# Performance work log

Hardware: AMD Instinct MI355X
Metric: run time of the kernel (lower is better)

## Reference

```python
import jax, jax.numpy as jnp
import numpy as np

B, N, R = 16, 512, 10
DE, DR, DOUT = 256, 64, 256

def setup_inputs() -> dict:
    key = jax.random.key(0)
    k1, k2, k3, k4 = jax.random.split(key, 4)
    node_features = jax.random.normal(k1, (B, N, DE), dtype=jnp.float32)
    relation_features = jax.random.normal(k2, (B, R, DR), dtype=jnp.float32)
    adj = jax.random.uniform(k3, (B, R, N, N), dtype=jnp.float32)
    in_dim = (DE + DR) * R
    bound = float(np.sqrt(6.0 / (in_dim + DOUT)))  # xavier_uniform
    W = jax.random.uniform(k4, (DOUT, in_dim), dtype=jnp.float32, minval=-bound, maxval=bound)
    bias = jnp.zeros((DOUT,), dtype=jnp.float32)
    return {"node_features": node_features, "relation_features": relation_features,
            "adj": adj, "W": W, "bias": bias}

def reference(node_features, relation_features, adj, W, bias):
    # adj: [B,R,N,N]; node_features: [B,N,De]; relation_features: [B,R,Dr]
    # Per relation r: bmm(adj[:,r], cat([node, rel_r broadcast], -1))
    # Node part: adj @ node_features for every relation at once.
    node_part = jnp.einsum('brnm,bmd->brnd', adj, node_features)      # [B,R,N,De]
    # Relation part: adj @ (rel_r repeated over rows) == rowsum(adj) * rel_r
    rel_part = adj.sum(axis=-1)[..., None] * relation_features[:, :, None, :]  # [B,R,N,Dr]
    supports = jnp.concatenate([node_part, rel_part], axis=-1)        # [B,R,N,De+Dr]
    supports = supports.transpose(0, 2, 1, 3).reshape(node_features.shape[0],
                                                      node_features.shape[1], -1)  # [B,N,R*(De+Dr)]
    return supports @ W.T + bias
```

## Files before the change

### kernel.cpp

```cpp
#include <hip/hip_runtime.h>
#include <stdint.h>

#define B_     16
#define N_     512
#define R_     10
#define DE_    256
#define DR_    64
#define DOUT_  256
#define INDIM_ 3200
#define BLK_   320
#define RN_    5120
#define SPLITS_ 4
#define CPS_    20

typedef __bf16          v8bf  __attribute__((ext_vector_type(8)));
typedef unsigned short  v8us  __attribute__((ext_vector_type(8)));
typedef unsigned short  v4us  __attribute__((ext_vector_type(4)));
typedef float           f32x4 __attribute__((ext_vector_type(4)));

static __device__ __forceinline__ unsigned short f2b(float f) {
  union { float f; unsigned u; } c; c.f = f;
  unsigned r = c.u + 0x7FFFu + ((c.u >> 16) & 1u);
  return (unsigned short)(r >> 16);
}

static __device__ __forceinline__ v8bf us2bf(v8us u) {
  union { v8us u; v8bf b; } c; c.u = u; return c.b;
}

static __device__ __forceinline__ void gl_lds16(const void* g, void* l) {
  __builtin_amdgcn_global_load_lds(
      (const __attribute__((address_space(1))) void*)g,
      (__attribute__((address_space(3))) void*)l, 16, 0, 0);
}

static __device__ __forceinline__ void waitv4() { asm volatile("s_waitcnt vmcnt(4)" ::: "memory"); }
static __device__ __forceinline__ void waitv0() { asm volatile("s_waitcnt vmcnt(0)" ::: "memory"); }
static __device__ __forceinline__ void waitl0() { asm volatile("s_waitcnt lgkmcnt(0)" ::: "memory"); }
#define SCHED0() __builtin_amdgcn_sched_barrier(0)

__global__ void prep_all(const float* __restrict__ nf, const float* __restrict__ W,
                         const float* __restrict__ rel,
                         unsigned short* __restrict__ nodeB,
                         unsigned short* __restrict__ WnB,
                         float* __restrict__ Uf) {
  const int bb = blockIdx.x;
  const int tid = threadIdx.x;
  if (bb < 256) {
    const size_t base = (size_t)bb * 8192;
#pragma unroll
    for (int p = 0; p < 4; ++p) {
      size_t off = base + (size_t)p * 2048 + (size_t)tid * 8;
      float4 x = *(const float4*)(nf + off);
      float4 y = *(const float4*)(nf + off + 4);
      v8us u;
      u[0] = f2b(x.x); u[1] = f2b(x.y); u[2] = f2b(x.z); u[3] = f2b(x.w);
      u[4] = f2b(y.x); u[5] = f2b(y.y); u[6] = f2b(y.z); u[7] = f2b(y.w);
      *(v8us*)(nodeB + off) = u;
    }
  } else if (bb < 896) {
    int idx = (bb - 256) * 1024 + tid * 4;
    int r = idx >> 16;
    int o = (idx >> 8) & 255;
    int d = idx & 255;
    float4 x = *(const float4*)(W + (size_t)o * INDIM_ + r * BLK_ + d);
    v4us u;
    u[0] = f2b(x.x); u[1] = f2b(x.y); u[2] = f2b(x.z); u[3] = f2b(x.w);
    *(v4us*)(WnB + idx) = u;
  } else {
    int idx = (bb - 896) * 256 + tid;
    int o  = idx & 255;
    int br = idx >> 8;
    int r  = br % R_;
    const float* rp = rel + (size_t)br * DR_;
    const float* wp = W + (size_t)o * INDIM_ + r * BLK_ + DE_;
    float v = 0.f;
#pragma unroll 8
    for (int d = 0; d < DR_; ++d) v += rp[d] * wp[d];
    Uf[idx] = v;
  }
}

__global__ void stageA_gemm(const unsigned short* __restrict__ nodeB,
                            const unsigned short* __restrict__ WnB,
                            const float* __restrict__ Uf,
                            unsigned short* __restrict__ Gp) {
  __shared__ unsigned short S[40960];
  unsigned short* NodeP = S;
  unsigned short* Wbuf  = S + 16384;
  unsigned short* Cb    = S + 32768;
  const int b  = blockIdx.x;
  const int o0 = blockIdx.y * 128;
  const int m0 = (blockIdx.z & 7) * 64;
  const int r0 = (blockIdx.z >> 3) * 5;
  const int tid  = threadIdx.x;
  const int lane = tid & 63;
  const int wave = tid >> 6;
  const int wm = wave >> 1, wn = wave & 1;
  const int quad = lane >> 4, l16 = lane & 15;
  const int srl = lane >> 3;
  const int skc = lane & 7;

  const unsigned short* Nb = nodeB + (size_t)b * (N_ * DE_);

#pragma unroll
  for (int p = 0; p < 4; ++p)
#pragma unroll
    for (int it = 0; it < 2; ++it) {
      int rowblk = it * 32 + wave * 8;
      int rl = rowblk + srl;
      int kc = skc ^ (rl & 7);
      gl_lds16(Nb + (size_t)(m0 + rl) * DE_ + p * 64 + kc * 8,
               NodeP + p * 4096 + rowblk * 64);
    }
  {
    const unsigned short* Wb = WnB + (size_t)r0 * (DOUT_ * DE_);
#pragma unroll
    for (int it = 0; it < 4; ++it) {
      int rowblk = it * 32 + wave * 8;
      int rl = rowblk + srl;
      int kc = skc ^ (rl & 7);
      gl_lds16(Wb + (size_t)(o0 + rl) * DE_ + kc * 8, Wbuf + rowblk * 64);
    }
  }
  __syncthreads();

  for (int rr = 0; rr < 5; ++rr) {
    const int r = r0 + rr;
    f32x4 acc[4][2];
#pragma unroll
    for (int i = 0; i < 4; ++i)
#pragma unroll
      for (int j = 0; j < 2; ++j) acc[i][j] = f32x4{0.f, 0.f, 0.f, 0.f};

#pragma unroll
    for (int t = 0; t < 4; ++t) {
      if (rr < 4 || t < 3) {
        const int nr = (t < 3) ? r : (r + 1);
        const int nt = (t < 3) ? (t + 1) : 0;
        const unsigned short* Wb = WnB + (size_t)nr * (DOUT_ * DE_);
        unsigned short* Wd = Wbuf + ((t + 1) & 1) * 8192;
#pragma unroll
        for (int it = 0; it < 4; ++it) {
          int rowblk = it * 32 + wave * 8;
          int rl = rowblk + srl;
          int kc = skc ^ (rl & 7);
          gl_lds16(Wb + (size_t)(o0 + rl) * DE_ + nt * 64 + kc * 8, Wd + rowblk * 64);
        }
      }
      const unsigned short* Wc = Wbuf + (t & 1) * 8192;
      const unsigned short* Np = NodeP + t * 4096;
#pragma unroll
      for (int ks = 0; ks < 2; ++ks) {
        const int kb = ks * 4;
        v8bf av[4], bv[2];
#pragma unroll
        for (int mi = 0; mi < 4; ++mi) {
          int m = wm * 64 + mi * 16 + l16;
          av[mi] = us2bf(*(const v8us*)(Wc + m * 64 + (((kb + quad) ^ (m & 7)) * 8)));
        }
#pragma unroll
        for (int ni = 0; ni < 2; ++ni) {
          int c = wn * 32 + ni * 16 + l16;
          bv[ni] = us2bf(*(const v8us*)(Np + c * 64 + (((kb + quad) ^ (c & 7)) * 8)));
        }
#pragma unroll
        for (int mi = 0; mi < 4; ++mi)
#pragma unroll
          for (int ni = 0; ni < 2; ++ni)
            acc[mi][ni] = __builtin_amdgcn_mfma_f32_16x16x32_bf16(av[mi], bv[ni], acc[mi][ni], 0, 0, 0);
      }
      __syncthreads();
    }

#pragma unroll
    for (int mi = 0; mi < 4; ++mi)
#pragma unroll
      for (int tt = 0; tt < 4; ++tt) {
        int o_loc = wm * 64 + mi * 16 + quad * 4 + tt;
        float u = Uf[((size_t)b * R_ + r) * DOUT_ + o0 + o_loc];
#pragma unroll
        for (int ni = 0; ni < 2; ++ni) {
          int m_loc = wn * 32 + ni * 16 + l16;
          Cb[o_loc * 64 + m_loc] = f2b(acc[mi][ni][tt] + u);
        }
      }
    __syncthreads();
#pragma unroll
    for (int p = 0; p < 4; ++p) {
      int idx16 = p * 2048 + tid * 8;
      int orow = idx16 >> 6;
      int moff = idx16 & 63;
      unsigned short* dst = Gp + ((size_t)(b * DOUT_ + o0 + orow)) * RN_ + r * N_ + m0 + moff;
      *(v8us*)dst = *(const v8us*)(Cb + idx16);
    }
    __syncthreads();
  }
}

__global__ __launch_bounds__(512, 1)
void stageB_gemm(const float* __restrict__ adj,
                 const unsigned short* __restrict__ Gp,
                 float* __restrict__ part) {
  __shared__ unsigned short SB[2 * 24576];
  const int b  = blockIdx.x;
  const int n0 = blockIdx.y * 128;
  const int sp = blockIdx.z;
  const int tid  = threadIdx.x;
  const int lane = tid & 63;
  const int wave = tid >> 6;
  const int wm = wave >> 2;
  const int wn = wave & 3;
  const int quad = lane >> 4, l16 = lane & 15;

  const float* Ab = adj + (size_t)b * (R_ * N_ * N_);
  const unsigned short* Gb = Gp + (size_t)b * (DOUT_ * RN_);

  f32x4 acc[4][4];
#pragma unroll
  for (int i = 0; i < 4; ++i)
#pragma unroll
    for (int j = 0; j < 4; ++j) acc[i][j] = f32x4{0.f, 0.f, 0.f, 0.f};

  const int ar0 = tid >> 3;
  const int ac8 = tid & 7;
  const int acs = ac8 ^ (ar0 & 7);
  const int brl = wave * 8 + (lane >> 3);
  const int bkc = lane & 7;
  const int c0 = sp * CPS_;

  float4 As0[4], As1[4];

#define ISSUE_B(slot, cc) do { \
    unsigned short* Bd = SB + (slot) * 24576 + 8192; \
    const int k0b = (cc) << 6; \
    _Pragma("unroll") \
    for (int s = 0; s < 4; ++s) { \
      int rl = s * 64 + brl; \
      int kc = bkc ^ (rl & 7); \
      gl_lds16(Gb + (size_t)rl * RN_ + k0b + kc * 8, Bd + (s * 64 + wave * 8) * 64); \
    } } while (0)

#define ISSUE_A(AR, cc) do { \
    const float* g = Ab + ((size_t)((cc) >> 3) * N_ + n0) * N_ + ((cc) & 7) * 64 \
                     + (size_t)ar0 * N_ + ac8 * 8; \
    AR[0] = *(const float4*)(g); \
    AR[1] = *(const float4*)(g + 4); \
    AR[2] = *(const float4*)(g + 64 * N_); \
    AR[3] = *(const float4*)(g + 64 * N_ + 4); } while (0)

#define CONV_A(AR, slot) do { \
    v8us u0, u1; \
    u0[0] = f2b(AR[0].x); u0[1] = f2b(AR[0].y); u0[2] = f2b(AR[0].z); u0[3] = f2b(AR[0].w); \
    u0[4] = f2b(AR[1].x); u0[5] = f2b(AR[1].y); u0[6] = f2b(AR[1].z); u0[7] = f2b(AR[1].w); \
    u1[0] = f2b(AR[2].x); u1[1] = f2b(AR[2].y); u1[2] = f2b(AR[2].z); u1[3] = f2b(AR[2].w); \
    u1[4] = f2b(AR[3].x); u1[5] = f2b(AR[3].y); u1[6] = f2b(AR[3].z); u1[7] = f2b(AR[3].w); \
    unsigned short* Ad = SB + (slot) * 24576; \
    *(v8us*)(Ad + ar0 * 64 + acs * 8) = u0; \
    *(v8us*)(Ad + (ar0 + 64) * 64 + acs * 8) = u1; } while (0)

#define COMPUTE(slot) do { \
    const unsigned short* Alc = SB + (slot) * 24576; \
    const unsigned short* Blc = Alc + 8192; \
    _Pragma("unroll") \
    for (int ks = 0; ks < 2; ++ks) { \
      const int kb = ks * 4; \
      v8bf av[4], bv[4]; \
      _Pragma("unroll") \
      for (int mi = 0; mi < 4; ++mi) { \
        int m = wm * 64 + mi * 16 + l16; \
        av[mi] = us2bf(*(const v8us*)(Alc + m * 64 + (((kb + quad) ^ (m & 7)) * 8))); \
      } \
      _Pragma("unroll") \
      for (int ni = 0; ni < 4; ++ni) { \
        int o = wn * 64 + ni * 16 + l16; \
        bv[ni] = us2bf(*(const v8us*)(Blc + o * 64 + (((kb + quad) ^ (o & 7)) * 8))); \
      } \
      _Pragma("unroll") \
      for (int mi = 0; mi < 4; ++mi) \
        _Pragma("unroll") \
        for (int ni = 0; ni < 4; ++ni) \
          acc[mi][ni] = __builtin_amdgcn_mfma_f32_16x16x32_bf16(av[mi], bv[ni], acc[mi][ni], 0, 0, 0); \
    } } while (0)

  ISSUE_A(As0, c0 + 0);
  ISSUE_B(0, c0 + 0);
  ISSUE_A(As1, c0 + 1);
  waitv4();
  SCHED0();
  CONV_A(As0, 0);
  waitl0();
  __builtin_amdgcn_s_barrier();

  for (int t = 0; t < CPS_; t += 2) {
    {
      ISSUE_B(1, c0 + t + 1);
      if (t + 2 < CPS_) ISSUE_A(As0, c0 + t + 2);
      SCHED0();
      COMPUTE(0);
      if (t + 2 < CPS_) waitv4();
      else              waitv0();
      SCHED0();
      CONV_A(As1, 1);
      waitl0();
      __builtin_amdgcn_s_barrier();
    }
    {
      if (t + 2 < CPS_) {
        ISSUE_B(0, c0 + t + 2);
        if (t + 3 < CPS_) ISSUE_A(As1, c0 + t + 3);
        SCHED0();
        COMPUTE(1);
        if (t + 3 < CPS_) waitv4();
        else              waitv0();
        SCHED0();
        CONV_A(As0, 0);
        waitl0();
        __builtin_amdgcn_s_barrier();
      } else {
        SCHED0();
        COMPUTE(1);
      }
    }
  }

#undef ISSUE_B
#undef ISSUE_A
#undef CONV_A
#undef COMPUTE

  float* pb = part + (((size_t)sp * B_ + b) * N_) * DOUT_;
#pragma unroll
  for (int mi = 0; mi < 4; ++mi)
#pragma unroll
    for (int t4 = 0; t4 < 4; ++t4) {
      int row = n0 + wm * 64 + mi * 16 + quad * 4 + t4;
#pragma unroll
      for (int ni = 0; ni < 4; ++ni) {
        int col = wn * 64 + ni * 16 + l16;
        pb[(size_t)row * DOUT_ + col] = acc[mi][ni][t4];
      }
    }
}

__global__ void reduce_out(const float* __restrict__ part, const float* __restrict__ bias,
                           float* __restrict__ out) {
  const size_t idx = (size_t)blockIdx.x * 256 + threadIdx.x;
  const size_t stride = (size_t)B_ * N_ * DOUT_ / 4;
  f32x4 a = *(const f32x4*)(bias + (idx & 63) * 4);
#pragma unroll
  for (int s = 0; s < SPLITS_; ++s) {
    f32x4 p = *(const f32x4*)((const float*)part + (stride * s + idx) * 4);
    a += p;
  }
  *(f32x4*)(out + idx * 4) = a;
}

extern "C" void kernel_launch(void* const* d_in, const int* in_sizes, int n_in,
                              void* d_out, int out_size, void* d_ws, size_t ws_size,
                              hipStream_t stream) {
  const float* node = (const float*)d_in[0];
  const float* rel  = (const float*)d_in[1];
  const float* adj  = (const float*)d_in[2];
  const float* W    = (const float*)d_in[3];
  const float* bias = (const float*)d_in[4];
  float* out = (float*)d_out;

  char* ws = (char*)d_ws;
  unsigned short* nodeB = (unsigned short*)(ws);
  unsigned short* WnB   = (unsigned short*)(ws + ((size_t)5 << 20));
  float*          Uf    = (float*)         (ws + ((size_t)7 << 20));
  unsigned short* Gp    = (unsigned short*)(ws + ((size_t)8 << 20));
  float*          part  = (float*)         (ws + ((size_t)48 << 20));

  prep_all<<<dim3(1056), 256, 0, stream>>>(node, W, rel, nodeB, WnB, Uf);
  stageA_gemm<<<dim3(B_, 2, 16), 256, 0, stream>>>(nodeB, WnB, Uf, Gp);
  stageB_gemm<<<dim3(B_, N_ / 128, SPLITS_), 512, 0, stream>>>(adj, Gp, part);
  reduce_out<<<dim3((B_ * N_ * DOUT_ / 4) / 256), 256, 0, stream>>>(part, bias, out);
}
```

Before: 289.5 us.

## Halve stageB K-tile, double split-K, allow two blocks per CU

```diff
diff --git a/kernel.cpp b/kernel.cpp
--- a/kernel.cpp
+++ b/kernel.cpp
@@ -10,8 +10,8 @@
 #define INDIM_ 3200
 #define BLK_   320
 #define RN_    5120
-#define SPLITS_ 4
-#define CPS_    20
+#define SPLITS_ 8
+#define STEPS_  20
 
 typedef __bf16          v8bf  __attribute__((ext_vector_type(8)));
 typedef unsigned short  v8us  __attribute__((ext_vector_type(8)));
@@ -33,11 +33,6 @@
       (const __attribute__((address_space(1))) void*)g,
       (__attribute__((address_space(3))) void*)l, 16, 0, 0);
 }
-
-static __device__ __forceinline__ void waitv4() { asm volatile("s_waitcnt vmcnt(4)" ::: "memory"); }
-static __device__ __forceinline__ void waitv0() { asm volatile("s_waitcnt vmcnt(0)" ::: "memory"); }
-static __device__ __forceinline__ void waitl0() { asm volatile("s_waitcnt lgkmcnt(0)" ::: "memory"); }
-#define SCHED0() __builtin_amdgcn_sched_barrier(0)
 
 __global__ void prep_all(const float* __restrict__ nf, const float* __restrict__ W,
                          const float* __restrict__ rel,
@@ -198,11 +193,11 @@
   }
 }
 
-__global__ __launch_bounds__(512, 1)
+__global__ __launch_bounds__(512, 2)
 void stageB_gemm(const float* __restrict__ adj,
                  const unsigned short* __restrict__ Gp,
                  float* __restrict__ part) {
-  __shared__ unsigned short SB[2 * 24576];
+  __shared__ unsigned short SB[2 * 13312];
   const int b  = blockIdx.x;
   const int n0 = blockIdx.y * 128;
   const int sp = blockIdx.z;
@@ -222,110 +217,78 @@
 #pragma unroll
     for (int j = 0; j < 4; ++j) acc[i][j] = f32x4{0.f, 0.f, 0.f, 0.f};
 
-  const int ar0 = tid >> 3;
-  const int ac8 = tid & 7;
-  const int acs = ac8 ^ (ar0 & 7);
-  const int brl = wave * 8 + (lane >> 3);
-  const int bkc = lane & 7;
-  const int c0 = sp * CPS_;
-
-  float4 As0[4], As1[4];
+  const int ar  = tid >> 2;
+  const int ac8 = tid & 3;
+  const int brl = (lane >> 2);
+  const int bkc = lane & 3;
+  const int c0 = sp * STEPS_;
 
 #define ISSUE_B(slot, cc) do { \
-    unsigned short* Bd = SB + (slot) * 24576 + 8192; \
-    const int k0b = (cc) << 6; \
+    unsigned short* Bd = SB + (slot) * 13312 + 5120; \
     _Pragma("unroll") \
-    for (int s = 0; s < 4; ++s) { \
-      int rl = s * 64 + brl; \
-      int kc = bkc ^ (rl & 7); \
-      gl_lds16(Gb + (size_t)rl * RN_ + k0b + kc * 8, Bd + (s * 64 + wave * 8) * 64); \
+    for (int s = 0; s < 2; ++s) { \
+      int gr = s * 128 + wave * 16 + brl; \
+      int kc = bkc ^ ((gr >> 1) & 3); \
+      gl_lds16(Gb + (size_t)gr * RN_ + (size_t)(cc) * 32 + kc * 8, \
+               Bd + (s * 128 + wave * 16) * 32); \
     } } while (0)
 
-#define ISSUE_A(AR, cc) do { \
-    const float* g = Ab + ((size_t)((cc) >> 3) * N_ + n0) * N_ + ((cc) & 7) * 64 \
-                     + (size_t)ar0 * N_ + ac8 * 8; \
-    AR[0] = *(const float4*)(g); \
-    AR[1] = *(const float4*)(g + 4); \
-    AR[2] = *(const float4*)(g + 64 * N_); \
-    AR[3] = *(const float4*)(g + 64 * N_ + 4); } while (0)
-
-#define CONV_A(AR, slot) do { \
-    v8us u0, u1; \
-    u0[0] = f2b(AR[0].x); u0[1] = f2b(AR[0].y); u0[2] = f2b(AR[0].z); u0[3] = f2b(AR[0].w); \
-    u0[4] = f2b(AR[1].x); u0[5] = f2b(AR[1].y); u0[6] = f2b(AR[1].z); u0[7] = f2b(AR[1].w); \
-    u1[0] = f2b(AR[2].x); u1[1] = f2b(AR[2].y); u1[2] = f2b(AR[2].z); u1[3] = f2b(AR[2].w); \
-    u1[4] = f2b(AR[3].x); u1[5] = f2b(AR[3].y); u1[6] = f2b(AR[3].z); u1[7] = f2b(AR[3].w); \
-    unsigned short* Ad = SB + (slot) * 24576; \
-    *(v8us*)(Ad + ar0 * 64 + acs * 8) = u0; \
-    *(v8us*)(Ad + (ar0 + 64) * 64 + acs * 8) = u1; } while (0)
+#define LOAD_A(cc) do { \
+    const float* g = Ab + ((size_t)((cc) >> 4) * N_ + n0 + ar) * N_ \
+                     + ((cc) & 15) * 32 + ac8 * 8; \
+    a0 = *(const float4*)(g); \
+    a1 = *(const float4*)(g + 4); } while (0)
+
+#define CONV_A(slot) do { \
+    v8us u; \
+    u[0] = f2b(a0.x); u[1] = f2b(a0.y); u[2] = f2b(a0.z); u[3] = f2b(a0.w); \
+    u[4] = f2b(a1.x); u[5] = f2b(a1.y); u[6] = f2b(a1.z); u[7] = f2b(a1.w); \
+    *(v8us*)(SB + (slot) * 13312 + ar * 40 + ac8 * 8) = u; } while (0)
 
 #define COMPUTE(slot) do { \
-    const unsigned short* Alc = SB + (slot) * 24576; \
-    const unsigned short* Blc = Alc + 8192; \
+    const unsigned short* Alc = SB + (slot) * 13312; \
+    const unsigned short* Blc = Alc + 5120; \
+    v8bf av[4], bv[4]; \
     _Pragma("unroll") \
-    for (int ks = 0; ks < 2; ++ks) { \
-      const int kb = ks * 4; \
-      v8bf av[4], bv[4]; \
+    for (int mi = 0; mi < 4; ++mi) { \
+      int m = wm * 64 + mi * 16 + l16; \
+      av[mi] = us2bf(*(const v8us*)(Alc + m * 40 + quad * 8)); \
+    } \
+    _Pragma("unroll") \
+    for (int ni = 0; ni < 4; ++ni) { \
+      int o = wn * 64 + ni * 16 + l16; \
+      bv[ni] = us2bf(*(const v8us*)(Blc + o * 32 + ((quad ^ ((o >> 1) & 3)) * 8))); \
+    } \
+    _Pragma("unroll") \
+    for (int mi = 0; mi < 4; ++mi) \
       _Pragma("unroll") \
-      for (int mi = 0; mi < 4; ++mi) { \
-        int m = wm * 64 + mi * 16 + l16; \
-        av[mi] = us2bf(*(const v8us*)(Alc + m * 64 + (((kb + quad) ^ (m & 7)) * 8))); \
-      } \
-      _Pragma("unroll") \
-      for (int ni = 0; ni < 4; ++ni) { \
-        int o = wn * 64 + ni * 16 + l16; \
-        bv[ni] = us2bf(*(const v8us*)(Blc + o * 64 + (((kb + quad) ^ (o & 7)) * 8))); \
-      } \
-      _Pragma("unroll") \
-      for (int mi = 0; mi < 4; ++mi) \
-        _Pragma("unroll") \
-        for (int ni = 0; ni < 4; ++ni) \
-          acc[mi][ni] = __builtin_amdgcn_mfma_f32_16x16x32_bf16(av[mi], bv[ni], acc[mi][ni], 0, 0, 0); \
-    } } while (0)
-
-  ISSUE_A(As0, c0 + 0);
-  ISSUE_B(0, c0 + 0);
-  ISSUE_A(As1, c0 + 1);
-  waitv4();
-  SCHED0();
-  CONV_A(As0, 0);
-  waitl0();
-  __builtin_amdgcn_s_barrier();
-
-  for (int t = 0; t < CPS_; t += 2) {
-    {
-      ISSUE_B(1, c0 + t + 1);
-      if (t + 2 < CPS_) ISSUE_A(As0, c0 + t + 2);
-      SCHED0();
-      COMPUTE(0);
-      if (t + 2 < CPS_) waitv4();
-      else              waitv0();
-      SCHED0();
-      CONV_A(As1, 1);
-      waitl0();
-      __builtin_amdgcn_s_barrier();
-    }
-    {
-      if (t + 2 < CPS_) {
-        ISSUE_B(0, c0 + t + 2);
-        if (t + 3 < CPS_) ISSUE_A(As1, c0 + t + 3);
-        SCHED0();
-        COMPUTE(1);
-        if (t + 3 < CPS_) waitv4();
-        else              waitv0();
-        SCHED0();
-        CONV_A(As0, 0);
-        waitl0();
-        __builtin_amdgcn_s_barrier();
-      } else {
-        SCHED0();
-        COMPUTE(1);
-      }
-    }
+      for (int ni = 0; ni < 4; ++ni) \
+        acc[mi][ni] = __builtin_amdgcn_mfma_f32_16x16x32_bf16(av[mi], bv[ni], acc[mi][ni], 0, 0, 0); \
+    } while (0)
+
+  {
+    float4 a0, a1;
+    ISSUE_B(0, c0);
+    LOAD_A(c0);
+    CONV_A(0);
+  }
+  __syncthreads();
+
+  for (int t = 0; t < STEPS_; ++t) {
+    const int cur = t & 1, nxt = cur ^ 1;
+    float4 a0, a1;
+    const bool pf = (t + 1 < STEPS_);
+    if (pf) {
+      ISSUE_B(nxt, c0 + t + 1);
+      LOAD_A(c0 + t + 1);
+    }
+    COMPUTE(cur);
+    if (pf) CONV_A(nxt);
+    __syncthreads();
   }
 
 #undef ISSUE_B
-#undef ISSUE_A
+#undef LOAD_A
 #undef CONV_A
 #undef COMPUTE
 
```

New measurement: 303.5 us. 1.05x slower.
